# Kernel optimization log

Hardware: AMD Instinct MI355X
Metric: run time of the kernel (lower is better)

The kernel has to match this reference:

```python
import jax, jax.numpy as jnp
import numpy as np

N_NODES = 100000
N_EDGES = 3200000
IN_Z = 32
PROJ_H = 64
LOOP_D = 32
DEC_H = 64


def setup_inputs() -> dict:
    key = jax.random.key(0)
    ks = jax.random.split(key, 10)
    z_mod = jax.random.normal(ks[0], (N_NODES, IN_Z), dtype=jnp.float32)
    edge_index = jax.random.randint(ks[1], (2, N_EDGES), 0, N_NODES, dtype=jnp.int64)
    # loop_proj: Linear(32->64), ReLU, Linear(64->32)
    w1 = jax.random.normal(ks[2], (IN_Z, PROJ_H), dtype=jnp.float32) / np.sqrt(IN_Z)
    b1 = jnp.zeros((PROJ_H,), dtype=jnp.float32)
    w2 = jax.random.normal(ks[3], (PROJ_H, LOOP_D), dtype=jnp.float32) / np.sqrt(PROJ_H)
    b2 = jnp.zeros((LOOP_D,), dtype=jnp.float32)
    # decoder: Linear(2*loop_dim -> dec_hidden), ReLU, Linear(dec_hidden -> 1)
    dw1 = jax.random.normal(ks[4], (2 * LOOP_D, DEC_H), dtype=jnp.float32) / np.sqrt(2 * LOOP_D)
    db1 = jnp.zeros((DEC_H,), dtype=jnp.float32)
    dw2 = jax.random.normal(ks[5], (DEC_H, 1), dtype=jnp.float32) / np.sqrt(DEC_H)
    db2 = jnp.zeros((1,), dtype=jnp.float32)
    return {"z_mod": z_mod, "edge_index": edge_index, "w1": w1, "b1": b1,
            "w2": w2, "b2": b2, "dw1": dw1, "db1": db1, "dw2": dw2, "db2": db2}


def reference(z_mod, edge_index, w1, b1, w2, b2, dw1, db1, dw2, db2):
    # loop_proj: z_mod -> z_loop  [N, loop_dim]
    h = jax.nn.relu(z_mod @ w1 + b1)
    z_loop = h @ w2 + b2
    # edge-wise decoder: gather, concat, MLP
    zi = z_loop[edge_index[0]]            # [E, loop_dim]
    zj = z_loop[edge_index[1]]            # [E, loop_dim]
    he = jnp.concatenate([zi, zj], axis=-1)  # [E, 2*loop_dim]
    he = jax.nn.relu(he @ dw1 + db1)         # [E, dec_hidden]
    logits = (he @ dw2 + db2)[..., 0]        # [E]
    return logits
```

## Files before the change

### kernel.cpp

```cpp
#include <hip/hip_runtime.h>


typedef short bfrag4 __attribute__((ext_vector_type(4)));
typedef short s16x8  __attribute__((ext_vector_type(8)));
typedef float f32x4v __attribute__((ext_vector_type(4)));

#define N_NODES 100000
#define N_EDGES 3200000

__device__ __forceinline__ unsigned short f2bf(float f) {
    unsigned int i = __float_as_uint(f);
    unsigned int r = i + 0x7FFFu + ((i >> 16) & 1u);
    return (unsigned short)(r >> 16);
}

__device__ __forceinline__ bfrag4 cvt4(float x0, float x1, float x2, float x3) {
    bfrag4 v;
    v[0] = (short)f2bf(x0);
    v[1] = (short)f2bf(x1);
    v[2] = (short)f2bf(x2);
    v[3] = (short)f2bf(x3);
    return v;
}

__device__ __forceinline__ s16x8 dq8(long g, float s) {
    int lo = (int)g;
    int hi = (int)(g >> 32);
    s16x8 o;
#pragma unroll
    for (int j = 0; j < 4; ++j) {
        int bj = (lo << (24 - 8 * j)) >> 24;
        o[j] = (short)f2bf((float)bj * s);
    }
#pragma unroll
    for (int j = 0; j < 4; ++j) {
        int bj = (hi << (24 - 8 * j)) >> 24;
        o[4 + j] = (short)f2bf((float)bj * s);
    }
    return o;
}

__global__ __launch_bounds__(256) void node_proj_kernel(
    const float* __restrict__ z_mod,
    const float* __restrict__ w1,
    const float* __restrict__ b1,
    const float* __restrict__ w2,
    const float* __restrict__ b2,
    char*  __restrict__ z8,
    float* __restrict__ scales)
{
    __shared__ unsigned short hbuf[4][16 * 72];

    const int tid  = threadIdx.x;
    const int wave = tid >> 6;
    const int lane = tid & 63;
    const int quad = lane >> 4;
    const int col  = lane & 15;

    bfrag4 bw1[2][4];
    float  bias1[4];
    for (int t = 0; t < 4; ++t) {
        const int n = col + 16 * t;
        for (int s = 0; s < 2; ++s)
            for (int j = 0; j < 4; ++j)
                bw1[s][t][j] = (short)f2bf(w1[(s * 16 + quad * 4 + j) * 64 + n]);
        bias1[t] = b1[n];
    }
    bfrag4 bw2[4][2];
    float  bias2[2];
    for (int t = 0; t < 2; ++t) {
        const int n = col + 16 * t;
        for (int s = 0; s < 4; ++s)
            for (int j = 0; j < 4; ++j)
                bw2[s][t][j] = (short)f2bf(w2[(s * 16 + quad * 4 + j) * 32 + n]);
        bias2[t] = b2[n];
    }

    unsigned short* hrow = &hbuf[wave][0];

    const int gwave  = blockIdx.x * 4 + wave;
    const int nwaves = gridDim.x * 4;
    const int ntiles = N_NODES / 16;

    for (int tile = gwave; tile < ntiles; tile += nwaves) {
        const int node0 = tile * 16;
        const float* zrow = z_mod + (size_t)(node0 + col) * 32;

        f32x4v za0 = *(const f32x4v*)(zrow + 0 * 16 + quad * 4);
        f32x4v za1 = *(const f32x4v*)(zrow + 1 * 16 + quad * 4);
        bfrag4 a10 = cvt4(za0[0], za0[1], za0[2], za0[3]);
        bfrag4 a11 = cvt4(za1[0], za1[1], za1[2], za1[3]);

        f32x4v acc[4];
        for (int t = 0; t < 4; ++t) {
            f32x4v c = {bias1[t], bias1[t], bias1[t], bias1[t]};
            c = __builtin_amdgcn_mfma_f32_16x16x16bf16_1k(a10, bw1[0][t], c, 0, 0, 0);
            c = __builtin_amdgcn_mfma_f32_16x16x16bf16_1k(a11, bw1[1][t], c, 0, 0, 0);
            acc[t] = c;
        }

        for (int t = 0; t < 4; ++t)
            for (int r = 0; r < 4; ++r) {
                float v = acc[t][r];
                v = v > 0.f ? v : 0.f;
                hrow[(quad * 4 + r) * 72 + (col + 16 * t)] = f2bf(v);
            }
        asm volatile("" ::: "memory");

        f32x4v acc2[2];
        for (int t = 0; t < 2; ++t)
            acc2[t] = (f32x4v){bias2[t], bias2[t], bias2[t], bias2[t]};
        for (int s = 0; s < 4; ++s) {
            bfrag4 a2 = *(const bfrag4*)(hrow + col * 72 + s * 16 + quad * 4);
            for (int t = 0; t < 2; ++t)
                acc2[t] = __builtin_amdgcn_mfma_f32_16x16x16bf16_1k(a2, bw2[s][t], acc2[t], 0, 0, 0);
        }
        asm volatile("" ::: "memory");

        float am[4];
        for (int r = 0; r < 4; ++r)
            am[r] = fmaxf(fabsf(acc2[0][r]), fabsf(acc2[1][r]));
        for (int mask = 1; mask <= 8; mask <<= 1)
            for (int r = 0; r < 4; ++r)
                am[r] = fmaxf(am[r], __shfl_xor(am[r], mask, 64));

        char* hb = (char*)hrow;
        for (int r = 0; r < 4; ++r) {
            const float inv = 127.f / fmaxf(am[r], 1e-30f);
            for (int t = 0; t < 2; ++t) {
                int q = (int)rintf(acc2[t][r] * inv);
                hb[(quad * 4 + r) * 32 + (col + 16 * t)] = (char)q;
            }
        }
        if (col == 0)
            for (int r = 0; r < 4; ++r)
                scales[node0 + quad * 4 + r] = am[r] * (1.f / 127.f);
        asm volatile("" ::: "memory");

        *(unsigned long long*)(z8 + (size_t)node0 * 32 + lane * 8) =
            *(const unsigned long long*)(hb + lane * 8);
        asm volatile("" ::: "memory");
    }
}

__global__ __launch_bounds__(256) void edge_dec_kernel(
    const int*   __restrict__ eidx,
    const char*  __restrict__ z8,
    const float* __restrict__ scales,
    const float* __restrict__ dw1,
    const float* __restrict__ db1,
    const float* __restrict__ dw2,
    const float* __restrict__ db2,
    float* __restrict__ out)
{
    const int tid  = threadIdx.x;
    const int lane = tid & 63;
    const int quad = lane >> 4;
    const int col  = lane & 15;

    s16x8 aw[2][4];
    f32x4v bias1v[4];
    float  w2v[4][4];
    for (int mt = 0; mt < 4; ++mt) {
        const int h = 16 * mt + col;
        for (int s = 0; s < 2; ++s)
            for (int j = 0; j < 8; ++j)
                aw[s][mt][j] = (short)f2bf(dw1[(32 * s + quad * 8 + j) * 64 + h]);
        for (int r = 0; r < 4; ++r) {
            bias1v[mt][r] = db1[16 * mt + quad * 4 + r];
            w2v[mt][r]    = dw2[16 * mt + quad * 4 + r];
        }
    }
    const float bias2 = db2[0];

    const int gwave  = blockIdx.x * 4 + (tid >> 6);
    const int nwaves = gridDim.x * 4;
    const int npairs = N_EDGES / 32;

    int sA = eidx[gwave * 32 + col];
    int sB = eidx[gwave * 32 + 16 + col];
    int dA = eidx[N_EDGES + gwave * 32 + col];
    int dB = eidx[N_EDGES + gwave * 32 + 16 + col];

    for (int p = gwave; p < npairs; p += nwaves) {
        const int e0 = p * 32;

        long gA0 = *(const long*)(z8 + ((size_t)sA << 5) + (quad << 3));
        long gA1 = *(const long*)(z8 + ((size_t)dA << 5) + (quad << 3));
        long gB0 = *(const long*)(z8 + ((size_t)sB << 5) + (quad << 3));
        long gB1 = *(const long*)(z8 + ((size_t)dB << 5) + (quad << 3));
        float scA0 = scales[sA];
        float scA1 = scales[dA];
        float scB0 = scales[sB];
        float scB1 = scales[dB];

        const int pn = p + nwaves;
        const int pc = pn < npairs ? pn : gwave;
        sA = eidx[pc * 32 + col];
        sB = eidx[pc * 32 + 16 + col];
        dA = eidx[N_EDGES + pc * 32 + col];
        dB = eidx[N_EDGES + pc * 32 + 16 + col];

        s16x8 fA0 = dq8(gA0, scA0);
        s16x8 fA1 = dq8(gA1, scA1);
        s16x8 fB0 = dq8(gB0, scB0);
        s16x8 fB1 = dq8(gB1, scB1);

        f32x4v accA[4], accB[4];
        for (int mt = 0; mt < 4; ++mt) {
            f32x4v c = __builtin_amdgcn_mfma_f32_16x16x32_bf16(aw[0][mt], fA0, bias1v[mt], 0, 0, 0);
            accA[mt] = __builtin_amdgcn_mfma_f32_16x16x32_bf16(aw[1][mt], fA1, c, 0, 0, 0);
        }
        for (int mt = 0; mt < 4; ++mt) {
            f32x4v c = __builtin_amdgcn_mfma_f32_16x16x32_bf16(aw[0][mt], fB0, bias1v[mt], 0, 0, 0);
            accB[mt] = __builtin_amdgcn_mfma_f32_16x16x32_bf16(aw[1][mt], fB1, c, 0, 0, 0);
        }

        float pA = 0.f, pB = 0.f;
        for (int mt = 0; mt < 4; ++mt)
            for (int r = 0; r < 4; ++r) {
                float vA = accA[mt][r]; vA = vA > 0.f ? vA : 0.f;
                float vB = accB[mt][r]; vB = vB > 0.f ? vB : 0.f;
                pA += vA * w2v[mt][r];
                pB += vB * w2v[mt][r];
            }
        pA += __shfl_xor(pA, 16, 64);
        pA += __shfl_xor(pA, 32, 64);
        pB += __shfl_xor(pB, 16, 64);
        pB += __shfl_xor(pB, 32, 64);

        if (lane < 32) {
            float v = (lane < 16 ? pA : pB) + bias2;
            out[e0 + lane] = v;
        }
    }
}

extern "C" void kernel_launch(void* const* d_in, const int* in_sizes, int n_in,
                              void* d_out, int out_size, void* d_ws, size_t ws_size,
                              hipStream_t stream) {
    const float* z_mod = (const float*)d_in[0];
    const int*   eidx  = (const int*)d_in[1];
    const float* w1    = (const float*)d_in[2];
    const float* b1    = (const float*)d_in[3];
    const float* w2    = (const float*)d_in[4];
    const float* b2    = (const float*)d_in[5];
    const float* dw1   = (const float*)d_in[6];
    const float* db1   = (const float*)d_in[7];
    const float* dw2   = (const float*)d_in[8];
    const float* db2   = (const float*)d_in[9];
    float* out = (float*)d_out;

    char*  z8     = (char*)d_ws;
    float* scales = (float*)((char*)d_ws + (size_t)N_NODES * 32);

    node_proj_kernel<<<512, 256, 0, stream>>>(z_mod, w1, b1, w2, b2, z8, scales);
    edge_dec_kernel<<<2048, 256, 0, stream>>>(eidx, z8, scales, dw1, db1, dw2, db2, out);
}
```

Before: 173.5 us.

## Gather node rows with 16-byte loads and redistribute via LDS

Each lane now fetches a 16-byte half of a source or destination node row, so two lanes cover one 32-byte int8 row, in place of four 8-byte gathers per lane. The data is staged through a per-wave shared-memory buffer and read back into the MFMA fragment layout. Scales are fetched with one coalesced load per lane and broadcast via shuffles, replacing four scattered scale loads. This cuts the number of global gather instructions and scale lookups, at the cost of LDS traffic and lacking explicit wave-level sync between the LDS write and read.

```diff
diff --git a/kernel.cpp b/kernel.cpp
--- a/kernel.cpp
+++ b/kernel.cpp
@@ -4,6 +4,7 @@
 typedef short bfrag4 __attribute__((ext_vector_type(4)));
 typedef short s16x8  __attribute__((ext_vector_type(8)));
 typedef float f32x4v __attribute__((ext_vector_type(4)));
+typedef int   i32x4  __attribute__((ext_vector_type(4)));
 
 #define N_NODES 100000
 #define N_EDGES 3200000
@@ -23,9 +24,9 @@
     return v;
 }
 
-__device__ __forceinline__ s16x8 dq8(long g, float s) {
-    int lo = (int)g;
-    int hi = (int)(g >> 32);
+__device__ __forceinline__ s16x8 dq16(long g, float s) {
+    const int lo = (int)g;
+    const int hi = (int)(g >> 32);
     s16x8 o;
 #pragma unroll
     for (int j = 0; j < 4; ++j) {
@@ -153,10 +154,17 @@
     const float* __restrict__ db2,
     float* __restrict__ out)
 {
+    __shared__ char xbuf[4][2][1024];
+
     const int tid  = threadIdx.x;
+    const int wave = tid >> 6;
     const int lane = tid & 63;
     const int quad = lane >> 4;
     const int col  = lane & 15;
+    const int eh   = lane >> 1;
+    const int hf   = lane & 1;
+    const int ss   = lane >> 5;
+    const int se   = lane & 31;
 
     s16x8 aw[2][4];
     f32x4v bias1v[4];
@@ -173,47 +181,58 @@
     }
     const float bias2 = db2[0];
 
-    const int gwave  = blockIdx.x * 4 + (tid >> 6);
+    const int gwave  = blockIdx.x * 4 + wave;
     const int nwaves = gridDim.x * 4;
     const int npairs = N_EDGES / 32;
 
-    int sA = eidx[gwave * 32 + col];
-    int sB = eidx[gwave * 32 + 16 + col];
-    int dA = eidx[N_EDGES + gwave * 32 + col];
-    int dB = eidx[N_EDGES + gwave * 32 + 16 + col];
+    char* wbS = &xbuf[wave][0][0];
+    char* wbD = &xbuf[wave][1][0];
+
+    const int rb = (2 * col + (quad >> 1)) * 16 + (quad & 1) * 8;
+
+    int iS = eidx[gwave * 32 + eh];
+    int iD = eidx[N_EDGES + gwave * 32 + eh];
+    int iC = eidx[ss * N_EDGES + gwave * 32 + se];
 
     for (int p = gwave; p < npairs; p += nwaves) {
         const int e0 = p * 32;
 
-        long gA0 = *(const long*)(z8 + ((size_t)sA << 5) + (quad << 3));
-        long gA1 = *(const long*)(z8 + ((size_t)dA << 5) + (quad << 3));
-        long gB0 = *(const long*)(z8 + ((size_t)sB << 5) + (quad << 3));
-        long gB1 = *(const long*)(z8 + ((size_t)dB << 5) + (quad << 3));
-        float scA0 = scales[sA];
-        float scA1 = scales[dA];
-        float scB0 = scales[sB];
-        float scB1 = scales[dB];
+        i32x4 vS = *(const i32x4*)(z8 + (size_t)iS * 32 + hf * 16);
+        i32x4 vD = *(const i32x4*)(z8 + (size_t)iD * 32 + hf * 16);
+        float sc = scales[iC];
 
         const int pn = p + nwaves;
         const int pc = pn < npairs ? pn : gwave;
-        sA = eidx[pc * 32 + col];
-        sB = eidx[pc * 32 + 16 + col];
-        dA = eidx[N_EDGES + pc * 32 + col];
-        dB = eidx[N_EDGES + pc * 32 + 16 + col];
-
-        s16x8 fA0 = dq8(gA0, scA0);
-        s16x8 fA1 = dq8(gA1, scA1);
-        s16x8 fB0 = dq8(gB0, scB0);
-        s16x8 fB1 = dq8(gB1, scB1);
+        iS = eidx[pc * 32 + eh];
+        iD = eidx[N_EDGES + pc * 32 + eh];
+        iC = eidx[ss * N_EDGES + pc * 32 + se];
+
+        *(i32x4*)(wbS + lane * 16) = vS;
+        *(i32x4*)(wbD + lane * 16) = vD;
+
+        long pSA = *(const long*)(wbS + rb);
+        long pSB = *(const long*)(wbS + 512 + rb);
+        long pDA = *(const long*)(wbD + rb);
+        long pDB = *(const long*)(wbD + 512 + rb);
+
+        float sA0 = __shfl(sc, col, 64);
+        float sB0 = __shfl(sc, 16 + col, 64);
+        float sA1 = __shfl(sc, 32 + col, 64);
+        float sB1 = __shfl(sc, 48 + col, 64);
+
+        s16x8 gA0 = dq16(pSA, sA0);
+        s16x8 gA1 = dq16(pDA, sA1);
+        s16x8 gB0 = dq16(pSB, sB0);
+        s16x8 gB1 = dq16(pDB, sB1);
 
         f32x4v accA[4], accB[4];
         for (int mt = 0; mt < 4; ++mt) {
-            f32x4v c = __builtin_amdgcn_mfma_f32_16x16x32_bf16(aw[0][mt], fA0, bias1v[mt], 0, 0, 0);
-            accA[mt] = __builtin_amdgcn_mfma_f32_16x16x32_bf16(aw[1][mt], fA1, c, 0, 0, 0);
+            f32x4v c = __builtin_amdgcn_mfma_f32_16x16x32_bf16(aw[0][mt], gA0, bias1v[mt], 0, 0, 0);
+            accA[mt] = __builtin_amdgcn_mfma_f32_16x16x32_bf16(aw[1][mt], gA1, c, 0, 0, 0);
         }
         for (int mt = 0; mt < 4; ++mt) {
-            f32x4v c = __builtin_amdgcn_mfma_f32_16x16x32_bf16(aw[0][mt], fB0, bias1v[mt], 0, 0, 0);
-            accB[mt] = __builtin_amdgcn_mfma_f32_16x16x32_bf16(aw[1][mt], fB1, c, 0, 0, 0);
+            f32x4v c = __builtin_amdgcn_mfma_f32_16x16x32_bf16(aw[0][mt], gB0, bias1v[mt], 0, 0, 0);
+            accB[mt] = __builtin_amdgcn_mfma_f32_16x16x32_bf16(aw[1][mt], gB1, c, 0, 0, 0);
         }
 
         float pA = 0.f, pB = 0.f;
```

Result: no change. 172.9 us (-0.4%).

## Share one bf16 scale per four nodes and cache scales in LDS

Applied to the files above, without the earlier changes.

The int8 node embeddings now use one shared scale per group of four nodes, stored as bf16, instead of a per-node fp32 scale. The whole 25k-entry scale table (about 50 KB) is copied into shared memory at the start of each edge block, so per-edge scale lookups become LDS reads rather than random global loads. The edge grid shrinks to 768 blocks, which fits the larger LDS footprint and spreads the preload cost over more work per block. Coarser scaling adds quantization error for nodes whose magnitude is much smaller than their group's maximum.

```diff
diff --git a/kernel.cpp b/kernel.cpp
--- a/kernel.cpp
+++ b/kernel.cpp
@@ -4,6 +4,7 @@
 typedef short bfrag4 __attribute__((ext_vector_type(4)));
 typedef short s16x8  __attribute__((ext_vector_type(8)));
 typedef float f32x4v __attribute__((ext_vector_type(4)));
+typedef int   i32x4  __attribute__((ext_vector_type(4)));
 
 #define N_NODES 100000
 #define N_EDGES 3200000
@@ -12,6 +13,11 @@
     unsigned int i = __float_as_uint(f);
     unsigned int r = i + 0x7FFFu + ((i >> 16) & 1u);
     return (unsigned short)(r >> 16);
+}
+
+__device__ __forceinline__ float bf2f(unsigned short b) {
+    unsigned int u = ((unsigned int)b) << 16;
+    return __uint_as_float(u);
 }
 
 __device__ __forceinline__ bfrag4 cvt4(float x0, float x1, float x2, float x3) {
@@ -24,8 +30,8 @@
 }
 
 __device__ __forceinline__ s16x8 dq8(long g, float s) {
-    int lo = (int)g;
-    int hi = (int)(g >> 32);
+    const int lo = (int)g;
+    const int hi = (int)(g >> 32);
     s16x8 o;
 #pragma unroll
     for (int j = 0; j < 4; ++j) {
@@ -46,8 +52,8 @@
     const float* __restrict__ b1,
     const float* __restrict__ w2,
     const float* __restrict__ b2,
-    char*  __restrict__ z8,
-    float* __restrict__ scales)
+    char*           __restrict__ z8,
+    unsigned short* __restrict__ scg)
 {
     __shared__ unsigned short hbuf[4][16 * 72];
 
@@ -123,18 +129,17 @@
         for (int mask = 1; mask <= 8; mask <<= 1)
             for (int r = 0; r < 4; ++r)
                 am[r] = fmaxf(am[r], __shfl_xor(am[r], mask, 64));
+        const float gm = fmaxf(fmaxf(am[0], am[1]), fmaxf(am[2], am[3]));
+        const float inv = 127.f / fmaxf(gm, 1e-30f);
 
         char* hb = (char*)hrow;
-        for (int r = 0; r < 4; ++r) {
-            const float inv = 127.f / fmaxf(am[r], 1e-30f);
+        for (int r = 0; r < 4; ++r)
             for (int t = 0; t < 2; ++t) {
                 int q = (int)rintf(acc2[t][r] * inv);
                 hb[(quad * 4 + r) * 32 + (col + 16 * t)] = (char)q;
             }
-        }
         if (col == 0)
-            for (int r = 0; r < 4; ++r)
-                scales[node0 + quad * 4 + r] = am[r] * (1.f / 127.f);
+            scg[(node0 >> 2) + quad] = f2bf(gm * (1.f / 127.f));
         asm volatile("" ::: "memory");
 
         *(unsigned long long*)(z8 + (size_t)node0 * 32 + lane * 8) =
@@ -144,19 +149,25 @@
 }
 
 __global__ __launch_bounds__(256) void edge_dec_kernel(
-    const int*   __restrict__ eidx,
-    const char*  __restrict__ z8,
-    const float* __restrict__ scales,
-    const float* __restrict__ dw1,
-    const float* __restrict__ db1,
-    const float* __restrict__ dw2,
-    const float* __restrict__ db2,
+    const int*            __restrict__ eidx,
+    const char*           __restrict__ z8,
+    const unsigned short* __restrict__ scg,
+    const float*          __restrict__ dw1,
+    const float*          __restrict__ db1,
+    const float*          __restrict__ dw2,
+    const float*          __restrict__ db2,
     float* __restrict__ out)
 {
+    __shared__ i32x4 slds4[3128];
+    unsigned short* slds = (unsigned short*)slds4;
+
     const int tid  = threadIdx.x;
     const int lane = tid & 63;
     const int quad = lane >> 4;
     const int col  = lane & 15;
+
+    for (int i = tid; i < 3128; i += 256)
+        slds4[i] = ((const i32x4*)scg)[i];
 
     s16x8 aw[2][4];
     f32x4v bias1v[4];
@@ -173,9 +184,13 @@
     }
     const float bias2 = db2[0];
 
+    __syncthreads();
+
     const int gwave  = blockIdx.x * 4 + (tid >> 6);
     const int nwaves = gridDim.x * 4;
     const int npairs = N_EDGES / 32;
+
+    const int qoff = quad * 8;
 
     int sA = eidx[gwave * 32 + col];
     int sB = eidx[gwave * 32 + 16 + col];
@@ -185,14 +200,15 @@
     for (int p = gwave; p < npairs; p += nwaves) {
         const int e0 = p * 32;
 
-        long gA0 = *(const long*)(z8 + ((size_t)sA << 5) + (quad << 3));
-        long gA1 = *(const long*)(z8 + ((size_t)dA << 5) + (quad << 3));
-        long gB0 = *(const long*)(z8 + ((size_t)sB << 5) + (quad << 3));
-        long gB1 = *(const long*)(z8 + ((size_t)dB << 5) + (quad << 3));
-        float scA0 = scales[sA];
-        float scA1 = scales[dA];
-        float scB0 = scales[sB];
-        float scB1 = scales[dB];
+        long gA0 = *(const long*)(z8 + sA * 32 + qoff);
+        long gA1 = *(const long*)(z8 + dA * 32 + qoff);
+        long gB0 = *(const long*)(z8 + sB * 32 + qoff);
+        long gB1 = *(const long*)(z8 + dB * 32 + qoff);
+
+        float scA0 = bf2f(slds[sA >> 2]);
+        float scA1 = bf2f(slds[dA >> 2]);
+        float scB0 = bf2f(slds[sB >> 2]);
+        float scB1 = bf2f(slds[dB >> 2]);
 
         const int pn = p + nwaves;
         const int pc = pn < npairs ? pn : gwave;
@@ -251,9 +267,9 @@
     const float* db2   = (const float*)d_in[9];
     float* out = (float*)d_out;
 
-    char*  z8     = (char*)d_ws;
-    float* scales = (float*)((char*)d_ws + (size_t)N_NODES * 32);
-
-    node_proj_kernel<<<512, 256, 0, stream>>>(z_mod, w1, b1, w2, b2, z8, scales);
-    edge_dec_kernel<<<2048, 256, 0, stream>>>(eidx, z8, scales, dw1, db1, dw2, db2, out);
-}
+    char*           z8  = (char*)d_ws;
+    unsigned short* scg = (unsigned short*)((char*)d_ws + (size_t)N_NODES * 32);
+
+    node_proj_kernel<<<512, 256, 0, stream>>>(z_mod, w1, b1, w2, b2, z8, scg);
+    edge_dec_kernel<<<768, 256, 0, stream>>>(eidx, z8, scg, dw1, db1, dw2, db2, out);
+}
```

After: 166.9 us. 1.04x faster.
